# Performance work log

Hardware: AMD Instinct MI355X
Metric: run time of the kernel (lower is better)

The kernel has to match this reference:

```python
import jax, jax.numpy as jnp
import numpy as np

# dims
B, N, T, F, D = 16, 64, 168, 8, 248   # batch, stations, seq, features, gcn_dim
E = D + F                              # transformer dmodel = 256
H = 8                                  # attention heads
FF = 4 * E                             # expansion_factor * dmodel


def _layer_norm(x, g, b, eps=1e-5):
    m = jnp.mean(x, axis=-1, keepdims=True)
    v = jnp.var(x, axis=-1, keepdims=True)
    return (x - m) * jax.lax.rsqrt(v + eps) * g + b


def setup_inputs() -> dict:
    key = jax.random.key(0)
    ks = jax.random.split(key, 20)
    s = 0.02
    return {
        'x': jax.random.normal(ks[0], (B, N, T, F), jnp.float32),
        'locs': jax.random.uniform(ks[1], (B, N, 2), jnp.float32),
        'pos_em': jax.random.normal(ks[2], (B, T, E), jnp.float32),
        'periodic_em': jax.random.normal(ks[3], (B, T, E), jnp.float32),
        'gcn_w': jax.random.normal(ks[4], (F, D), jnp.float32) * s,
        'gcn_b': jnp.zeros((D,), jnp.float32),
        'fc1_w': jax.random.normal(ks[5], (D, D), jnp.float32) * s,
        'fc1_b': jnp.zeros((D,), jnp.float32),
        'wq': jax.random.normal(ks[6], (E, E), jnp.float32) * s,
        'bq': jnp.zeros((E,), jnp.float32),
        'wk': jax.random.normal(ks[7], (E, E), jnp.float32) * s,
        'bk': jnp.zeros((E,), jnp.float32),
        'wv': jax.random.normal(ks[8], (E, E), jnp.float32) * s,
        'bv': jnp.zeros((E,), jnp.float32),
        'wo': jax.random.normal(ks[9], (E, E), jnp.float32) * s,
        'bo': jnp.zeros((E,), jnp.float32),
        'ln1_g': jnp.ones((E,), jnp.float32),
        'ln1_b': jnp.zeros((E,), jnp.float32),
        'ln2_g': jnp.ones((E,), jnp.float32),
        'ln2_b': jnp.zeros((E,), jnp.float32),
        'ff1_w': jax.random.normal(ks[10], (E, FF), jnp.float32) * s,
        'ff1_b': jnp.zeros((FF,), jnp.float32),
        'ff2_w': jax.random.normal(ks[11], (FF, E), jnp.float32) * s,
        'ff2_b': jnp.zeros((E,), jnp.float32),
    }


def reference(x, locs, pos_em, periodic_em, gcn_w, gcn_b, fc1_w, fc1_b,
              wq, bq, wk, bk, wv, bv, wo, bo,
              ln1_g, ln1_b, ln2_g, ln2_b, ff1_w, ff1_b, ff2_w, ff2_b):
    b, n, t, f = x.shape
    # --- inverse-distance-weighted dense adjacency (fully connected graph) ---
    diff = locs[:, :, None, :] - locs[:, None, :, :]            # [B,N,N,2]
    dist = jnp.sqrt(jnp.sum(diff * diff, -1) + 1e-12)           # [B,N,N]
    w = jnp.where(jnp.eye(n, dtype=bool), 0.0, 1.0 / dist)      # no self edges
    w = w / jnp.sum(w, -1, keepdims=True)                       # norm=True
    # --- GCNConv (self loops + symmetric normalization), batched over B and T ---
    a = w + jnp.eye(n, dtype=x.dtype)
    dinv = jax.lax.rsqrt(jnp.sum(a, -1))
    a = a * dinv[:, :, None] * dinv[:, None, :]                 # [B,N,N]
    h = jnp.einsum('bntf,fd->bntd', x, gcn_w)                   # xW
    g = jax.nn.relu(jnp.einsum('bmn,bntd->bmtd', a, h) + gcn_b) # aggregate + relu
    g = jnp.einsum('bntd,de->bnte', g, fc1_w) + fc1_b           # fc1
    # --- concat features, flatten stations into batch, add positional embedding ---
    tok = jnp.concatenate([x, g], -1).reshape(b * n, t, -1)     # [B*N,T,E]
    tok = tok + jnp.repeat(pos_em, n, axis=0)                   # dropout=identity (eval)
    per = jnp.repeat(periodic_em, n, axis=0)
    # --- transformer encoder layer (periodic embedding conditions Q/K) ---
    e = tok.shape[-1]
    dh = e // H
    qk_in = tok + per
    q = (qk_in @ wq + bq).reshape(b * n, t, H, dh)
    k = (qk_in @ wk + bk).reshape(b * n, t, H, dh)
    v = (tok @ wv + bv).reshape(b * n, t, H, dh)
    s = jnp.einsum('bthd,bshd->bhts', q, k) * (1.0 / float(np.sqrt(dh)))
    p = jax.nn.softmax(s, axis=-1)
    o = jnp.einsum('bhts,bshd->bthd', p, v).reshape(b * n, t, e)
    o = o @ wo + bo
    h1 = _layer_norm(tok + o, ln1_g, ln1_b)
    ff = jax.nn.relu(h1 @ ff1_w + ff1_b) @ ff2_w + ff2_b
    out = _layer_norm(h1 + ff, ln2_g, ln2_b)
    return out.reshape(b, n, t, e)
```

## Files before the change

kernel.cpp:

```cpp
#include <hip/hip_runtime.h>
#include <hip/hip_bf16.h>

constexpr int B_  = 16;
constexpr int N_  = 64;
constexpr int T_  = 168;
constexpr int F_  = 8;
constexpr int E_  = 256;
constexpr int H_  = 8;
constexpr int DH_ = 32;
constexpr int NT_ = N_ * T_;
constexpr int LDQ_ = 768;

typedef __bf16 bf16x8 __attribute__((ext_vector_type(8)));
typedef float  f32x4  __attribute__((ext_vector_type(4)));
typedef float  f32x4u __attribute__((ext_vector_type(4), aligned(4)));

__device__ __forceinline__ unsigned short f2b(float f) {
  union { float f; unsigned int u; } v; v.f = f;
  unsigned int r = (v.u + 0x7FFFu + ((v.u >> 16) & 1u)) >> 16;
  return (unsigned short)r;
}
__device__ __forceinline__ float b2f(unsigned short h) {
  union { unsigned int u; float f; } v; v.u = ((unsigned int)h) << 16;
  return v.f;
}
__device__ __forceinline__ unsigned int cvtpk(float lo, float hi) {
  unsigned int r;
  asm("v_cvt_pk_bf16_f32 %0, %1, %2" : "=v"(r) : "v"(lo), "v"(hi));
  return r;
}
__device__ __forceinline__ void gload16(const void* g, void* l) {
  __builtin_amdgcn_global_load_lds(
      (const __attribute__((address_space(1))) unsigned int*)g,
      (__attribute__((address_space(3))) unsigned int*)l, 16, 0, 0);
}

__global__ void adj_kernel(const float* __restrict__ locs, float* __restrict__ a) {
  int b = blockIdx.x;
  int m = threadIdx.x;
  __shared__ float lx[64], ly[64];
  lx[m] = locs[(b * 64 + m) * 2 + 0];
  ly[m] = locs[(b * 64 + m) * 2 + 1];
  __syncthreads();
  float x = lx[m], y = ly[m];
  float sum = 0.f;
  for (int n = 0; n < 64; ++n) {
    float dx = x - lx[n], dy = y - ly[n];
    float d = sqrtf(dx * dx + dy * dy + 1e-12f);
    sum += (n == m) ? 0.f : 1.f / d;
  }
  float inv = 0.5f / sum;
  for (int n = 0; n < 64; ++n) {
    float dx = x - lx[n], dy = y - ly[n];
    float d = sqrtf(dx * dx + dy * dy + 1e-12f);
    float w = (n == m) ? 0.5f : inv / d;
    a[(b * 64 + m) * 64 + n] = w;
  }
}

__global__ void convw_kernel(const float* __restrict__ in, unsigned short* __restrict__ outT,
                             int K, int N, int Kp, int Np) {
  int idx = blockIdx.x * 256 + threadIdx.x;
  if (idx >= Np * Kp) return;
  int n = idx / Kp, k = idx % Kp;
  float v = (k < K && n < N) ? in[(long)k * N + n] : 0.f;
  outT[idx] = f2b(v);
}

__global__ __launch_bounds__(256) void gcn_kernel(
    const float* __restrict__ x, const float* __restrict__ adj,
    const float* __restrict__ gcn_w, const float* __restrict__ gcn_b,
    const float* __restrict__ pos_em, const float* __restrict__ per_em,
    unsigned short* __restrict__ G, unsigned short* __restrict__ tokb,
    unsigned short* __restrict__ qkb, int b0) {
  int bl = blockIdx.x / T_;
  int t = blockIdx.x % T_;
  int b = b0 + bl;
  int tid = threadIdx.x;
  __shared__ float sX[512];
  __shared__ float sXA[512];
  const float* adjb = adj + b * 4096;
  for (int i = tid; i < 512; i += 256) {
    int n = i >> 3, f = i & 7;
    sX[i] = x[((long)(b * 64 + n) * T_ + t) * F_ + f];
  }
  __syncthreads();
  for (int i = tid; i < 512; i += 256) {
    int m = i >> 3, f = i & 7;
    float s = 0.f;
    for (int n = 0; n < 64; ++n) s += adjb[(m << 6) + n] * sX[(n << 3) + f];
    sXA[i] = s;
  }
  {
    long pbase = ((long)bl * T_ + t) * E_;
    for (int i = tid; i < 512; i += 256) {
      int m = i >> 3, f = i & 7;
      long lrow = (long)(bl * 64 + m) * T_ + t;
      float base = sX[i] + pos_em[pbase + f];
      tokb[lrow * E_ + f] = f2b(base);
      qkb[lrow * E_ + f]  = f2b(base + per_em[pbase + f]);
    }
  }
  __syncthreads();
  for (int i = tid; i < 64 * 256; i += 256) {
    int m = i >> 8, d = i & 255;
    float v = 0.f;
    if (d < 248) {
      float s = gcn_b[d];
      const float* xam = &sXA[m << 3];
#pragma unroll
      for (int f = 0; f < 8; ++f) s += xam[f] * gcn_w[f * 248 + d];
      v = fmaxf(s, 0.f);
    }
    long lrow = (long)(bl * 64 + m) * T_ + t;
    G[lrow * 256 + d] = f2b(v);
  }
}

template <int KCHUNKS, int WAVES>
__global__ __launch_bounds__(WAVES * 64) void block_gemm(
    const unsigned short* __restrict__ A, int lda,
    const unsigned short* __restrict__ Bt, int K, int Nact,
    const float* __restrict__ bias,
    float* Cf, unsigned short* Cb1, unsigned short* Cb2,
    const float* __restrict__ emb1, const float* __restrict__ emb2,
    const unsigned short* __restrict__ resb, const float* resf,
    int c0, int ldc, int relu) {
  __shared__ unsigned short As[64 * 256];
  const int tid = threadIdx.x;
  const int lane = tid & 63, w = tid >> 6;
  const int l15 = lane & 15, lg = lane >> 4;
  const int m0 = blockIdx.x * 64;
  const int n0w = blockIdx.y * (WAVES * 64) + w * 64;

  f32x4 acc[4][4];
#pragma unroll
  for (int i = 0; i < 4; ++i)
#pragma unroll
    for (int j = 0; j < 4; ++j) acc[i][j] = (f32x4){0.f, 0.f, 0.f, 0.f};

  for (int kc = 0; kc < KCHUNKS; ++kc) {
    if (kc) __syncthreads();
#pragma unroll
    for (int j = 0; j < 32 / WAVES; ++j) {
      int idx = j * (WAVES * 64) + tid;
      int row = idx >> 5, g = idx & 31;
      int swg = (g & 24) | ((g & 7) ^ (row & 7));
      gload16(A + (long)(m0 + row) * lda + kc * 256 + swg * 8,
              &As[(j * (WAVES * 64) + w * 64) * 8]);
    }
    bf16x8 Wa[4], Wb[4], Xf[4];
    auto ldw = [&](bf16x8 (&W)[4], int ks) {
#pragma unroll
      for (int nf = 0; nf < 4; ++nf)
        W[nf] = *reinterpret_cast<const bf16x8*>(
            Bt + (long)(n0w + nf * 16 + l15) * K + kc * 256 + ks * 32 + (lg << 3));
    };
    auto ldx = [&](int ks) {
#pragma unroll
      for (int mf = 0; mf < 4; ++mf) {
        int row = (mf << 4) + l15;
        int ksg = (ks << 2) + lg;
        int sw = (ksg & 24) | ((ksg & 7) ^ (row & 7));
        Xf[mf] = *reinterpret_cast<const bf16x8*>(&As[((row << 5) + sw) * 8]);
      }
    };
    auto mm = [&](bf16x8 (&W)[4]) {
      __builtin_amdgcn_s_setprio(1);
#pragma unroll
      for (int mf = 0; mf < 4; ++mf)
#pragma unroll
        for (int nf = 0; nf < 4; ++nf)
          acc[mf][nf] = __builtin_amdgcn_mfma_f32_16x16x32_bf16(W[nf], Xf[mf], acc[mf][nf], 0, 0, 0);
      __builtin_amdgcn_s_setprio(0);
    };
    ldw(Wa, 0);
    asm volatile("s_waitcnt vmcnt(0)" ::: "memory");
    __syncthreads();
#pragma unroll
    for (int kp = 0; kp < 4; ++kp) {
      ldw(Wb, kp * 2 + 1);
      ldx(kp * 2);
      mm(Wa);
      if (kp < 3) ldw(Wa, kp * 2 + 2);
      ldx(kp * 2 + 1);
      mm(Wb);
    }
  }

  const int cb = lg << 2;
#pragma unroll
  for (int mf = 0; mf < 4; ++mf) {
    int rr = m0 + (mf << 4) + l15;
    int ar = (rr / NT_) * T_ + (rr % T_);
    long rbase  = (long)rr * ldc + c0;
    long rbase2 = (long)rr * 256 + c0;
    long abase  = (long)ar * 256 + c0;
#pragma unroll
    for (int nf = 0; nf < 4; ++nf) {
      int gcol = n0w + (nf << 4) + cb;
      if (gcol < Nact) {
        float v0 = acc[mf][nf][0], v1 = acc[mf][nf][1];
        float v2 = acc[mf][nf][2], v3 = acc[mf][nf][3];
        if (bias) {
          f32x4u b4 = *reinterpret_cast<const f32x4u*>(bias + gcol);
          v0 += b4[0]; v1 += b4[1]; v2 += b4[2]; v3 += b4[3];
        }
        if (relu) {
          v0 = fmaxf(v0, 0.f); v1 = fmaxf(v1, 0.f);
          v2 = fmaxf(v2, 0.f); v3 = fmaxf(v3, 0.f);
        }
        if (resb) {
          ushort4 rv = *reinterpret_cast<const ushort4*>(resb + rbase2 + gcol);
          v0 += b2f(rv.x); v1 += b2f(rv.y); v2 += b2f(rv.z); v3 += b2f(rv.w);
        }
        if (resf) {
          f32x4u r4 = *reinterpret_cast<const f32x4u*>(resf + rbase + gcol);
          v0 += r4[0]; v1 += r4[1]; v2 += r4[2]; v3 += r4[3];
        }
        if (emb1) {
          f32x4u e4 = *reinterpret_cast<const f32x4u*>(emb1 + abase + gcol);
          v0 += e4[0]; v1 += e4[1]; v2 += e4[2]; v3 += e4[3];
        }
        if (Cf) {
          f32x4u o; o[0] = v0; o[1] = v1; o[2] = v2; o[3] = v3;
          *reinterpret_cast<f32x4u*>(Cf + rbase + gcol) = o;
        }
        if (Cb1) {
          uint2 p = {cvtpk(v0, v1), cvtpk(v2, v3)};
          *reinterpret_cast<uint2*>(Cb1 + rbase + gcol) = p;
        }
        if (Cb2) {
          f32x4u e4 = *reinterpret_cast<const f32x4u*>(emb2 + abase + gcol);
          uint2 p = {cvtpk(v0 + e4[0], v1 + e4[1]), cvtpk(v2 + e4[2], v3 + e4[3])};
          *reinterpret_cast<uint2*>(Cb2 + rbase + gcol) = p;
        }
      }
    }
  }
}

__global__ __launch_bounds__(256) void wo_ln_kernel(
    const unsigned short* __restrict__ A, int lda,
    const unsigned short* __restrict__ Wt,
    const float* __restrict__ bias,
    const unsigned short* __restrict__ resb,
    const float* __restrict__ lng, const float* __restrict__ lnb,
    unsigned short* __restrict__ outb) {
  __shared__ unsigned short As[64 * 256];
  __shared__ float red[4][4][16][2];
  const int tid = threadIdx.x;
  const int lane = tid & 63, w = tid >> 6;
  const int l15 = lane & 15, lg = lane >> 4;
  const int m0 = blockIdx.x * 64;
  const int n0w = w * 64;

  f32x4 acc[4][4];
#pragma unroll
  for (int i = 0; i < 4; ++i)
#pragma unroll
    for (int j = 0; j < 4; ++j) acc[i][j] = (f32x4){0.f, 0.f, 0.f, 0.f};

#pragma unroll
  for (int j = 0; j < 8; ++j) {
    int idx = j * 256 + tid;
    int row = idx >> 5, g = idx & 31;
    int swg = (g & 24) | ((g & 7) ^ (row & 7));
    gload16(A + (long)(m0 + row) * lda + swg * 8, &As[(j * 256 + w * 64) * 8]);
  }
  bf16x8 Wa[4], Wb[4], Xf[4];
  auto ldw = [&](bf16x8 (&W)[4], int ks) {
#pragma unroll
    for (int nf = 0; nf < 4; ++nf)
      W[nf] = *reinterpret_cast<const bf16x8*>(
          Wt + (long)(n0w + nf * 16 + l15) * 256 + ks * 32 + (lg << 3));
  };
  auto ldx = [&](int ks) {
#pragma unroll
    for (int mf = 0; mf < 4; ++mf) {
      int row = (mf << 4) + l15;
      int ksg = (ks << 2) + lg;
      int sw = (ksg & 24) | ((ksg & 7) ^ (row & 7));
      Xf[mf] = *reinterpret_cast<const bf16x8*>(&As[((row << 5) + sw) * 8]);
    }
  };
  auto mm = [&](bf16x8 (&W)[4]) {
    __builtin_amdgcn_s_setprio(1);
#pragma unroll
    for (int mf = 0; mf < 4; ++mf)
// ... 25 lines not shown
#pragma unroll
    for (int nf = 0; nf < 4; ++nf) {
      int gcol = n0w + (nf << 4) + cb;
      f32x4u b4 = *reinterpret_cast<const f32x4u*>(bias + gcol);
      ushort4 rv = *reinterpret_cast<const ushort4*>(resb + rbase2 + gcol);
      float v0 = acc[mf][nf][0] + b4[0] + b2f(rv.x);
      float v1 = acc[mf][nf][1] + b4[1] + b2f(rv.y);
      float v2 = acc[mf][nf][2] + b4[2] + b2f(rv.z);
      float v3 = acc[mf][nf][3] + b4[3] + b2f(rv.w);
      acc[mf][nf][0] = v0; acc[mf][nf][1] = v1;
      acc[mf][nf][2] = v2; acc[mf][nf][3] = v3;
      s[mf] += v0 + v1 + v2 + v3;
      s2[mf] += v0 * v0 + v1 * v1 + v2 * v2 + v3 * v3;
    }
    s[mf] += __shfl_xor(s[mf], 16, 64);
    s[mf] += __shfl_xor(s[mf], 32, 64);
    s2[mf] += __shfl_xor(s2[mf], 16, 64);
    s2[mf] += __shfl_xor(s2[mf], 32, 64);
    if (lg == 0) { red[w][mf][l15][0] = s[mf]; red[w][mf][l15][1] = s2[mf]; }
  }
  __syncthreads();
#pragma unroll
  for (int mf = 0; mf < 4; ++mf) {
    float S  = red[0][mf][l15][0] + red[1][mf][l15][0] + red[2][mf][l15][0] + red[3][mf][l15][0];
    float S2 = red[0][mf][l15][1] + red[1][mf][l15][1] + red[2][mf][l15][1] + red[3][mf][l15][1];
    float mean = S * 0.00390625f;
    float var = S2 * 0.00390625f - mean * mean;
    float rs = rsqrtf(var + 1e-5f);
    int rr = m0 + (mf << 4) + l15;
    long rbase = (long)rr * 256;
#pragma unroll
    for (int nf = 0; nf < 4; ++nf) {
      int gcol = n0w + (nf << 4) + cb;
      f32x4u g4 = *reinterpret_cast<const f32x4u*>(lng + gcol);
      f32x4u t4 = *reinterpret_cast<const f32x4u*>(lnb + gcol);
      float o0 = (acc[mf][nf][0] - mean) * rs * g4[0] + t4[0];
      float o1 = (acc[mf][nf][1] - mean) * rs * g4[1] + t4[1];
      float o2 = (acc[mf][nf][2] - mean) * rs * g4[2] + t4[2];
      float o3 = (acc[mf][nf][3] - mean) * rs * g4[3] + t4[3];
      uint2 p = {cvtpk(o0, o1), cvtpk(o2, o3)};
      *reinterpret_cast<uint2*>(outb + rbase + gcol) = p;
    }
  }
}

__global__ __launch_bounds__(512, 4) void ff_fused_kernel(
    const unsigned short* __restrict__ h1,
    const unsigned short* __restrict__ W1,
    const unsigned short* __restrict__ W2,
    const float* __restrict__ b1, const float* __restrict__ b2,
    const float* __restrict__ lng, const float* __restrict__ lnb,
    float* __restrict__ out) {
  __shared__ unsigned short h1s[64 * 256];
  __shared__ unsigned short fis[64 * 128];
  __shared__ float red[8][4][16][2];
  const int tid = threadIdx.x;
  const int lane = tid & 63, w = tid >> 6;
  const int l15 = lane & 15, lg = lane >> 4;
  const int m0 = blockIdx.x * 64;

#pragma unroll
  for (int j = 0; j < 4; ++j) {
    int idx = j * 512 + tid;
    int row = idx >> 5, g = idx & 31;
    int swg = (g & 24) | ((g & 7) ^ (row & 7));
    gload16(h1 + (long)(m0 + row) * 256 + swg * 8, &h1s[(j * 512 + w * 64) * 8]);
  }

  f32x4 acc2[4][2];
#pragma unroll
  for (int i = 0; i < 4; ++i)
#pragma unroll
    for (int j = 0; j < 2; ++j) acc2[i][j] = (f32x4){0.f, 0.f, 0.f, 0.f};

  bf16x8 W1a, W1b, W2a[2], W2b[2], Xf[4];
  auto ldw1 = [&](bf16x8& W, int hc, int ks) {
    W = *reinterpret_cast<const bf16x8*>(
        W1 + (long)(hc * 128 + w * 16 + l15) * 256 + ks * 32 + (lg << 3));
  };
  auto ldw2 = [&](bf16x8 (&W)[2], int hc, int ks) {
#pragma unroll
    for (int nf = 0; nf < 2; ++nf)
      W[nf] = *reinterpret_cast<const bf16x8*>(
          W2 + (long)(w * 32 + nf * 16 + l15) * 1024 + hc * 128 + ks * 32 + (lg << 3));
  };
  auto ldxh = [&](int ks) {
#pragma unroll
    for (int mf = 0; mf < 4; ++mf) {
      int row = (mf << 4) + l15;
      int ksg = (ks << 2) + lg;
      int sw = (ksg & 24) | ((ksg & 7) ^ (row & 7));
      Xf[mf] = *reinterpret_cast<const bf16x8*>(&h1s[((row << 5) + sw) * 8]);
    }
  };
  auto ldxf = [&](int ks) {
#pragma unroll
    for (int mf = 0; mf < 4; ++mf) {
      int row = (mf << 4) + l15;
      int ksg = (ks << 2) + lg;
      int sw = (ksg & 8) | ((ksg & 7) ^ (row & 7));
      Xf[mf] = *reinterpret_cast<const bf16x8*>(&fis[((row << 4) + sw) * 8]);
    }
  };

  const int cb = lg << 2;
  bool first = true;
  for (int hc = 0; hc < 8; ++hc) {
    f32x4 acc1[4];
#pragma unroll
    for (int i = 0; i < 4; ++i) acc1[i] = (f32x4){0.f, 0.f, 0.f, 0.f};
    ldw1(W1a, hc, 0);
    if (first) {
      asm volatile("s_waitcnt vmcnt(1)" ::: "memory");
      __syncthreads();
      first = false;
    }
#pragma unroll
    for (int kp = 0; kp < 4; ++kp) {
      ldw1(W1b, hc, kp * 2 + 1);
      ldxh(kp * 2);
      __builtin_amdgcn_s_setprio(1);
#pragma unroll
      for (int mf = 0; mf < 4; ++mf)
        acc1[mf] = __builtin_amdgcn_mfma_f32_16x16x32_bf16(W1a, Xf[mf], acc1[mf], 0, 0, 0);
      __builtin_amdgcn_s_setprio(0);
      if (kp < 3) ldw1(W1a, hc, kp * 2 + 2);
      ldxh(kp * 2 + 1);
      __builtin_amdgcn_s_setprio(1);
#pragma unroll
      for (int mf = 0; mf < 4; ++mf)
        acc1[mf] = __builtin_amdgcn_mfma_f32_16x16x32_bf16(W1b, Xf[mf], acc1[mf], 0, 0, 0);
      __builtin_amdgcn_s_setprio(0);
    }
    if (hc) __syncthreads();
#pragma unroll
    for (int mf = 0; mf < 4; ++mf) {
      int row = (mf << 4) + l15;
      int col = w * 16 + cb;
      f32x4u b4 = *reinterpret_cast<const f32x4u*>(b1 + hc * 128 + col);
      float v0 = fmaxf(acc1[mf][0] + b4[0], 0.f);
      float v1 = fmaxf(acc1[mf][1] + b4[1], 0.f);
      float v2 = fmaxf(acc1[mf][2] + b4[2], 0.f);
      float v3 = fmaxf(acc1[mf][3] + b4[3], 0.f);
      int g = col >> 3;
      int swg = (g & 8) | ((g & 7) ^ (row & 7));
      uint2 p = {cvtpk(v0, v1), cvtpk(v2, v3)};
      *reinterpret_cast<uint2*>(&fis[((row << 4) + swg) * 8 + (col & 7)]) = p;
    }
    ldw2(W2a, hc, 0);
    __syncthreads();
#pragma unroll
    for (int kp = 0; kp < 2; ++kp) {
      ldw2(W2b, hc, kp * 2 + 1);
      ldxf(kp * 2);
      __builtin_amdgcn_s_setprio(1);
#pragma unroll
      for (int mf = 0; mf < 4; ++mf)
#pragma unroll
        for (int nf = 0; nf < 2; ++nf)
          acc2[mf][nf] = __builtin_amdgcn_mfma_f32_16x16x32_bf16(W2a[nf], Xf[mf], acc2[mf][nf], 0, 0, 0);
      __builtin_amdgcn_s_setprio(0);
      if (kp < 1) ldw2(W2a, hc, kp * 2 + 2);
      ldxf(kp * 2 + 1);
      __builtin_amdgcn_s_setprio(1);
#pragma unroll
      for (int mf = 0; mf < 4; ++mf)
#pragma unroll
        for (int nf = 0; nf < 2; ++nf)
          acc2[mf][nf] = __builtin_amdgcn_mfma_f32_16x16x32_bf16(W2b[nf], Xf[mf], acc2[mf][nf], 0, 0, 0);
      __builtin_amdgcn_s_setprio(0);
    }
  }

  float s[4], s2[4];
#pragma unroll
  for (int mf = 0; mf < 4; ++mf) {
    int row = (mf << 4) + l15;
    s[mf] = 0.f; s2[mf] = 0.f;
#pragma unroll
    for (int nf = 0; nf < 2; ++nf) {
      int gcol = w * 32 + (nf << 4) + cb;
      f32x4u b4 = *reinterpret_cast<const f32x4u*>(b2 + gcol);
      int g = gcol >> 3;
      int swg = (g & 24) | ((g & 7) ^ (row & 7));
      ushort4 rv = *reinterpret_cast<const ushort4*>(&h1s[((row << 5) + swg) * 8 + (gcol & 7)]);
      float v0 = acc2[mf][nf][0] + b4[0] + b2f(rv.x);
      float v1 = acc2[mf][nf][1] + b4[1] + b2f(rv.y);
      float v2 = acc2[mf][nf][2] + b4[2] + b2f(rv.z);
      float v3 = acc2[mf][nf][3] + b4[3] + b2f(rv.w);
      acc2[mf][nf][0] = v0; acc2[mf][nf][1] = v1;
      acc2[mf][nf][2] = v2; acc2[mf][nf][3] = v3;
      s[mf] += v0 + v1 + v2 + v3;
      s2[mf] += v0 * v0 + v1 * v1 + v2 * v2 + v3 * v3;
    }
    s[mf] += __shfl_xor(s[mf], 16, 64);
    s[mf] += __shfl_xor(s[mf], 32, 64);
    s2[mf] += __shfl_xor(s2[mf], 16, 64);
    s2[mf] += __shfl_xor(s2[mf], 32, 64);
    if (lg == 0) { red[w][mf][l15][0] = s[mf]; red[w][mf][l15][1] = s2[mf]; }
  }
  __syncthreads();
#pragma unroll
  for (int mf = 0; mf < 4; ++mf) {
    float S = 0.f, S2 = 0.f;
#pragma unroll
    for (int ww = 0; ww < 8; ++ww) { S += red[ww][mf][l15][0]; S2 += red[ww][mf][l15][1]; }
    float mean = S * 0.00390625f;
    float var = S2 * 0.00390625f - mean * mean;
    float rs = rsqrtf(var + 1e-5f);
    int rr = m0 + (mf << 4) + l15;
    long rbase = (long)rr * 256;
#pragma unroll
    for (int nf = 0; nf < 2; ++nf) {
      int gcol = w * 32 + (nf << 4) + cb;
      f32x4u g4 = *reinterpret_cast<const f32x4u*>(lng + gcol);
      f32x4u t4 = *reinterpret_cast<const f32x4u*>(lnb + gcol);
      f32x4u o;
      o[0] = (acc2[mf][nf][0] - mean) * rs * g4[0] + t4[0];
      o[1] = (acc2[mf][nf][1] - mean) * rs * g4[1] + t4[1];
      o[2] = (acc2[mf][nf][2] - mean) * rs * g4[2] + t4[2];
      o[3] = (acc2[mf][nf][3] - mean) * rs * g4[3] + t4[3];
      *reinterpret_cast<f32x4u*>(out + rbase + gcol) = o;
    }
// ... 82 lines not shown
    f32x4 o0 = (f32x4){0.f, 0.f, 0.f, 0.f};
    f32x4 o1 = (f32x4){0.f, 0.f, 0.f, 0.f};
#pragma unroll
    for (int ks = 0; ks < 6; ++ks) {
      bf16x8 pf = *reinterpret_cast<const bf16x8*>(&Pw[l15 * 200 + ks * 32 + (lg << 3)]);
      bf16x8 v0 = *reinterpret_cast<const bf16x8*>(&VT[l15][ks * 32 + (lg << 3)]);
      bf16x8 v1 = *reinterpret_cast<const bf16x8*>(&VT[16 + l15][ks * 32 + (lg << 3)]);
      o0 = __builtin_amdgcn_mfma_f32_16x16x32_bf16(pf, v0, o0, 0, 0, 0);
      o1 = __builtin_amdgcn_mfma_f32_16x16x32_bf16(pf, v1, o1, 0, 0, 0);
    }
    int rg = lg << 2;
#pragma unroll
    for (int r = 0; r < 4; ++r) {
      int q = qt * 16 + rg + r;
      if (q < T_) {
        long ob = (long)q * LDQ_;
        O[ob + l15]      = f2b(o0[r] * inv_l[r]);
        O[ob + 16 + l15] = f2b(o1[r] * inv_l[r]);
      }
    }
  }
}

extern "C" void kernel_launch(void* const* d_in, const int* in_sizes, int n_in,
                              void* d_out, int out_size, void* d_ws, size_t ws_size,
                              hipStream_t stream) {
  const float* x      = (const float*)d_in[0];
  const float* locs   = (const float*)d_in[1];
  const float* pos_em = (const float*)d_in[2];
  const float* per_em = (const float*)d_in[3];
  const float* gcn_w  = (const float*)d_in[4];
  const float* gcn_b  = (const float*)d_in[5];
  const float* fc1_w  = (const float*)d_in[6];
  const float* fc1_b  = (const float*)d_in[7];
  const float* wq = (const float*)d_in[8];
  const float* bq = (const float*)d_in[9];
  const float* wk = (const float*)d_in[10];
  const float* bk = (const float*)d_in[11];
  const float* wv = (const float*)d_in[12];
  const float* bv = (const float*)d_in[13];
  const float* wo = (const float*)d_in[14];
  const float* bo = (const float*)d_in[15];
  const float* ln1_g = (const float*)d_in[16];
  const float* ln1_b = (const float*)d_in[17];
  const float* ln2_g = (const float*)d_in[18];
  const float* ln2_b = (const float*)d_in[19];
  const float* ff1_w = (const float*)d_in[20];
  const float* ff1_b = (const float*)d_in[21];
  const float* ff2_w = (const float*)d_in[22];
  const float* ff2_b = (const float*)d_in[23];
  float* out = (float*)d_out;

  const size_t ADJ_BYTES = 1u << 20;
  const size_t WB_BYTES  = 2u << 20;
  int CB = 16;
  while (CB > 1) {
    if (ADJ_BYTES + WB_BYTES + (size_t)CB * NT_ * 2560 <= ws_size) break;
    CB >>= 1;
  }
  char* ws = (char*)d_ws;
  float* adj = (float*)ws;
  unsigned short* wslab = (unsigned short*)(ws + ADJ_BYTES);
  unsigned short* fc1T  = wslab;
  unsigned short* wqkT  = wslab + 65536;
  unsigned short* wkT   = wslab + 2 * 65536;
  unsigned short* wvT   = wslab + 3 * 65536;
  unsigned short* woT   = wslab + 4 * 65536;
  unsigned short* ff1T  = wslab + 5 * 65536;
  unsigned short* ff2T  = wslab + 5 * 65536 + 262144;
  float* bqk = (float*)(ws + ADJ_BYTES + 1900544);

  unsigned short* tokb = (unsigned short*)(ws + ADJ_BYTES + WB_BYTES);
  unsigned short* qkb  = tokb + (size_t)CB * NT_ * 256;
  unsigned short* qkv  = qkb + (size_t)CB * NT_ * 256;
  unsigned short* h1b  = tokb;

  adj_kernel<<<B_, 64, 0, stream>>>(locs, adj);
  convw_kernel<<<256, 256, 0, stream>>>(fc1_w, fc1T, 248, 248, 256, 256);
  convw_kernel<<<256, 256, 0, stream>>>(wq, wqkT, 256, 256, 256, 256);
  convw_kernel<<<256, 256, 0, stream>>>(wk, wkT, 256, 256, 256, 256);
  convw_kernel<<<256, 256, 0, stream>>>(wv, wvT, 256, 256, 256, 256);
  convw_kernel<<<256, 256, 0, stream>>>(wo, woT, 256, 256, 256, 256);
  convw_kernel<<<1024, 256, 0, stream>>>(ff1_w, ff1T, 256, 1024, 256, 1024);
  convw_kernel<<<1024, 256, 0, stream>>>(ff2_w, ff2T, 1024, 256, 1024, 256);
  hipMemcpyAsync(bqk, bq, 256 * sizeof(float), hipMemcpyDeviceToDevice, stream);
  hipMemcpyAsync(bqk + 256, bk, 256 * sizeof(float), hipMemcpyDeviceToDevice, stream);

  for (int b0 = 0; b0 < B_; b0 += CB) {
    const int rows = CB * NT_;
    const int GX = rows / 64;
    const float* pos_c = pos_em + (long)b0 * T_ * E_;
    const float* per_c = per_em + (long)b0 * T_ * E_;
    float* out_c = out + (long)b0 * NT_ * E_;
    unsigned short* G = qkv;

    gcn_kernel<<<CB * T_, 256, 0, stream>>>(x, adj, gcn_w, gcn_b, pos_c, per_c,
                                            G, tokb, qkb, b0);
    block_gemm<1, 4><<<dim3(GX, 1), 256, 0, stream>>>(
        G, 256, fc1T, 256, 248, fc1_b, nullptr, tokb, qkb, pos_c, per_c,
        nullptr, nullptr, 8, 256, 0);
    block_gemm<1, 8><<<dim3(GX, 1), 512, 0, stream>>>(
        qkb, 256, wqkT, 256, 512, bqk, nullptr, qkv, nullptr, nullptr, nullptr,
        nullptr, nullptr, 0, LDQ_, 0);
    block_gemm<1, 4><<<dim3(GX, 1), 256, 0, stream>>>(
        tokb, 256, wvT, 256, 256, bv, nullptr, qkv, nullptr, nullptr, nullptr,
        nullptr, nullptr, 512, LDQ_, 0);
    attn_mfma_kernel<<<CB * N_ * H_, 256, 0, stream>>>(qkv);
    wo_ln_kernel<<<GX, 256, 0, stream>>>(qkv, LDQ_, woT, bo, tokb,
                                         ln1_g, ln1_b, h1b);
    ff_fused_kernel<<<GX, 512, 0, stream>>>(h1b, ff1T, ff2T, ff1_b, ff2_b,
                                            ln2_g, ln2_b, out_c);
  }
}
```

Baseline: 1.153 ms.

## Double-buffer FF intermediate tile to overlap first and second GEMM stages

The fused feed-forward kernel now keeps two LDS buffers for the ReLU intermediate. It computes the next hidden chunk's first GEMM while running the second GEMM on the current chunk, which cuts the per-chunk barriers from two to one. The goal is to hide latency by interleaving independent MFMA work between the two GEMMs. In exchange it uses an extra 16KB of LDS, raises register pressure from the live accumulators, and fully unrolls the loop, so occupancy may drop.

Result: no change. 1.173 ms (median of 2 runs) (+1.7%).

```diff
diff --git a/kernel.cpp b/kernel.cpp
--- a/kernel.cpp
+++ b/kernel.cpp
@@ -366,12 +366,14 @@
     const float* __restrict__ lng, const float* __restrict__ lnb,
     float* __restrict__ out) {
   __shared__ unsigned short h1s[64 * 256];
-  __shared__ unsigned short fis[64 * 128];
+  __shared__ unsigned short fisA[64 * 128];
+  __shared__ unsigned short fisB[64 * 128];
   __shared__ float red[8][4][16][2];
   const int tid = threadIdx.x;
   const int lane = tid & 63, w = tid >> 6;
   const int l15 = lane & 15, lg = lane >> 4;
   const int m0 = blockIdx.x * 64;
+  const int cb = lg << 2;
 
 #pragma unroll
   for (int j = 0; j < 4; ++j) {
@@ -380,6 +382,8 @@
     int swg = (g & 24) | ((g & 7) ^ (row & 7));
     gload16(h1 + (long)(m0 + row) * 256 + swg * 8, &h1s[(j * 512 + w * 64) * 8]);
   }
+  asm volatile("s_waitcnt vmcnt(0)" ::: "memory");
+  __syncthreads();
 
   f32x4 acc2[4][2];
 #pragma unroll
@@ -387,102 +391,97 @@
 #pragma unroll
     for (int j = 0; j < 2; ++j) acc2[i][j] = (f32x4){0.f, 0.f, 0.f, 0.f};
 
-  bf16x8 W1a, W1b, W2a[2], W2b[2], Xf[4];
   auto ldw1 = [&](bf16x8& W, int hc, int ks) {
     W = *reinterpret_cast<const bf16x8*>(
         W1 + (long)(hc * 128 + w * 16 + l15) * 256 + ks * 32 + (lg << 3));
   };
-  auto ldw2 = [&](bf16x8 (&W)[2], int hc, int ks) {
-#pragma unroll
-    for (int nf = 0; nf < 2; ++nf)
-      W[nf] = *reinterpret_cast<const bf16x8*>(
-          W2 + (long)(w * 32 + nf * 16 + l15) * 1024 + hc * 128 + ks * 32 + (lg << 3));
+  auto stage1 = [&](f32x4 (&a1)[4], int hc) {
+#pragma unroll
+    for (int i = 0; i < 4; ++i) a1[i] = (f32x4){0.f, 0.f, 0.f, 0.f};
+    bf16x8 Wa, Wb, Xf[4];
+    auto ldxh = [&](int ks) {
+#pragma unroll
+      for (int mf = 0; mf < 4; ++mf) {
+        int row = (mf << 4) + l15;
+        int ksg = (ks << 2) + lg;
+        int sw = (ksg & 24) | ((ksg & 7) ^ (row & 7));
+        Xf[mf] = *reinterpret_cast<const bf16x8*>(&h1s[((row << 5) + sw) * 8]);
+      }
+    };
+    ldw1(Wa, hc, 0);
+#pragma unroll
+    for (int kp = 0; kp < 4; ++kp) {
+      ldw1(Wb, hc, kp * 2 + 1);
+      ldxh(kp * 2);
+      __builtin_amdgcn_s_setprio(1);
+#pragma unroll
+      for (int mf = 0; mf < 4; ++mf)
+        a1[mf] = __builtin_amdgcn_mfma_f32_16x16x32_bf16(Wa, Xf[mf], a1[mf], 0, 0, 0);
+      __builtin_amdgcn_s_setprio(0);
+      if (kp < 3) ldw1(Wa, hc, kp * 2 + 2);
+      ldxh(kp * 2 + 1);
+      __builtin_amdgcn_s_setprio(1);
+#pragma unroll
+      for (int mf = 0; mf < 4; ++mf)
+        a1[mf] = __builtin_amdgcn_mfma_f32_16x16x32_bf16(Wb, Xf[mf], a1[mf], 0, 0, 0);
+      __builtin_amdgcn_s_setprio(0);
+    }
   };
-  auto ldxh = [&](int ks) {
+  auto stage2 = [&](const unsigned short* fis, int hc) {
+    bf16x8 Wf[2], Xf[4];
+#pragma unroll
+    for (int ks = 0; ks < 4; ++ks) {
+#pragma unroll
+      for (int nf = 0; nf < 2; ++nf)
+        Wf[nf] = *reinterpret_cast<const bf16x8*>(
+            W2 + (long)(w * 32 + nf * 16 + l15) * 1024 + hc * 128 + ks * 32 + (lg << 3));
+#pragma unroll
+      for (int mf = 0; mf < 4; ++mf) {
+        int row = (mf << 4) + l15;
+        int ksg = (ks << 2) + lg;
+        int sw = (ksg & 8) | ((ksg & 7) ^ (row & 7));
+        Xf[mf] = *reinterpret_cast<const bf16x8*>(&fis[((row << 4) + sw) * 8]);
+      }
+      __builtin_amdgcn_s_setprio(1);
+#pragma unroll
+      for (int mf = 0; mf < 4; ++mf)
+#pragma unroll
+        for (int nf = 0; nf < 2; ++nf)
+          acc2[mf][nf] = __builtin_amdgcn_mfma_f32_16x16x32_bf16(Wf[nf], Xf[mf], acc2[mf][nf], 0, 0, 0);
+      __builtin_amdgcn_s_setprio(0);
+    }
+  };
+  auto writeFis = [&](unsigned short* fis, f32x4 (&a1)[4], int hc) {
+    int col = w * 16 + cb;
+    f32x4u b4 = *reinterpret_cast<const f32x4u*>(b1 + hc * 128 + col);
+    int g = col >> 3;
 #pragma unroll
     for (int mf = 0; mf < 4; ++mf) {
       int row = (mf << 4) + l15;
-      int ksg = (ks << 2) + lg;
-      int sw = (ksg & 24) | ((ksg & 7) ^ (row & 7));
-      Xf[mf] = *reinterpret_cast<const bf16x8*>(&h1s[((row << 5) + sw) * 8]);
-    }
-  };
-  auto ldxf = [&](int ks) {
-#pragma unroll
-    for (int mf = 0; mf < 4; ++mf) {
-      int row = (mf << 4) + l15;
-      int ksg = (ks << 2) + lg;
-      int sw = (ksg & 8) | ((ksg & 7) ^ (row & 7));
-      Xf[mf] = *reinterpret_cast<const bf16x8*>(&fis[((row << 4) + sw) * 8]);
-    }
-  };
-
-  const int cb = lg << 2;
-  bool first = true;
-  for (int hc = 0; hc < 8; ++hc) {
-    f32x4 acc1[4];
-#pragma unroll
-    for (int i = 0; i < 4; ++i) acc1[i] = (f32x4){0.f, 0.f, 0.f, 0.f};
-    ldw1(W1a, hc, 0);
-    if (first) {
-      asm volatile("s_waitcnt vmcnt(1)" ::: "memory");
-      __syncthreads();
-      first = false;
-    }
-#pragma unroll
-    for (int kp = 0; kp < 4; ++kp) {
-      ldw1(W1b, hc, kp * 2 + 1);
-      ldxh(kp * 2);
-      __builtin_amdgcn_s_setprio(1);
-#pragma unroll
-      for (int mf = 0; mf < 4; ++mf)
-        acc1[mf] = __builtin_amdgcn_mfma_f32_16x16x32_bf16(W1a, Xf[mf], acc1[mf], 0, 0, 0);
-      __builtin_amdgcn_s_setprio(0);
-      if (kp < 3) ldw1(W1a, hc, kp * 2 + 2);
-      ldxh(kp * 2 + 1);
-      __builtin_amdgcn_s_setprio(1);
-#pragma unroll
-      for (int mf = 0; mf < 4; ++mf)
-        acc1[mf] = __builtin_amdgcn_mfma_f32_16x16x32_bf16(W1b, Xf[mf], acc1[mf], 0, 0, 0);
-      __builtin_amdgcn_s_setprio(0);
-    }
-    if (hc) __syncthreads();
-#pragma unroll
-    for (int mf = 0; mf < 4; ++mf) {
-      int row = (mf << 4) + l15;
-      int col = w * 16 + cb;
-      f32x4u b4 = *reinterpret_cast<const f32x4u*>(b1 + hc * 128 + col);
-      float v0 = fmaxf(acc1[mf][0] + b4[0], 0.f);
-      float v1 = fmaxf(acc1[mf][1] + b4[1], 0.f);
-      float v2 = fmaxf(acc1[mf][2] + b4[2], 0.f);
-      float v3 = fmaxf(acc1[mf][3] + b4[3], 0.f);
-      int g = col >> 3;
+      float v0 = fmaxf(a1[mf][0] + b4[0], 0.f);
+      float v1 = fmaxf(a1[mf][1] + b4[1], 0.f);
+      float v2 = fmaxf(a1[mf][2] + b4[2], 0.f);
+      float v3 = fmaxf(a1[mf][3] + b4[3], 0.f);
       int swg = (g & 8) | ((g & 7) ^ (row & 7));
       uint2 p = {cvtpk(v0, v1), cvtpk(v2, v3)};
       *reinterpret_cast<uint2*>(&fis[((row << 4) + swg) * 8 + (col & 7)]) = p;
     }
-    ldw2(W2a, hc, 0);
-    __syncthreads();
-#pragma unroll
-    for (int kp = 0; kp < 2; ++kp) {
-      ldw2(W2b, hc, kp * 2 + 1);
-      ldxf(kp * 2);
-      __builtin_amdgcn_s_setprio(1);
-#pragma unroll
-      for (int mf = 0; mf < 4; ++mf)
-#pragma unroll
-        for (int nf = 0; nf < 2; ++nf)
-          acc2[mf][nf] = __builtin_amdgcn_mfma_f32_16x16x32_bf16(W2a[nf], Xf[mf], acc2[mf][nf], 0, 0, 0);
-      __builtin_amdgcn_s_setprio(0);
-      if (kp < 1) ldw2(W2a, hc, kp * 2 + 2);
-      ldxf(kp * 2 + 1);
-      __builtin_amdgcn_s_setprio(1);
-#pragma unroll
-      for (int mf = 0; mf < 4; ++mf)
-#pragma unroll
-        for (int nf = 0; nf < 2; ++nf)
-          acc2[mf][nf] = __builtin_amdgcn_mfma_f32_16x16x32_bf16(W2b[nf], Xf[mf], acc2[mf][nf], 0, 0, 0);
-      __builtin_amdgcn_s_setprio(0);
+  };
+
+  f32x4 a1[4];
+  stage1(a1, 0);
+  writeFis(fisA, a1, 0);
+  __syncthreads();
+
+#pragma unroll
+  for (int hc = 0; hc < 8; ++hc) {
+    const unsigned short* rdp = (hc & 1) ? fisB : fisA;
+    unsigned short* wrp = (hc & 1) ? fisA : fisB;
+    if (hc < 7) stage1(a1, hc + 1);
+    stage2(rdp, hc);
+    if (hc < 7) {
+      writeFis(wrp, a1, hc + 1);
+      __syncthreads();
     }
   }
 
```

## Precompute periodic-embedding QK projection once per time step; restructure FF loop

Applied to the files above, without the earlier changes.

Uses linearity, (tok+per)Wq = tok·Wq + per·Wq, to compute per·[Wq|Wk]+bias once over B*T rows instead of B*N*T rows. The result is added as an fp32 embedding in the QK GEMM epilogue, which removes the separate qkb buffer and its writes. The fused FF kernel now processes two 128-wide hidden chunks per iteration with double-buffered LDS, halving the number of barriers. This adds an extra fp32 read of the perq table per QK output and more registers and LDS in the FF kernel.

New measurement: 1.197 ms. +3.8%, slower.

```diff
diff --git a/kernel.cpp b/kernel.cpp
--- a/kernel.cpp
+++ b/kernel.cpp
@@ -10,6 +10,7 @@
 constexpr int DH_ = 32;
 constexpr int NT_ = N_ * T_;
 constexpr int LDQ_ = 768;
+constexpr int BT_ = B_ * T_;
 
 typedef __bf16 bf16x8 __attribute__((ext_vector_type(8)));
 typedef float  f32x4  __attribute__((ext_vector_type(4)));
@@ -67,12 +68,17 @@
   outT[idx] = f2b(v);
 }
 
+__global__ void cvtb_kernel(const float* __restrict__ in, unsigned short* __restrict__ out,
+                            int n) {
+  int i = blockIdx.x * 256 + threadIdx.x;
+  if (i < n) out[i] = f2b(in[i]);
+}
+
 __global__ __launch_bounds__(256) void gcn_kernel(
     const float* __restrict__ x, const float* __restrict__ adj,
     const float* __restrict__ gcn_w, const float* __restrict__ gcn_b,
-    const float* __restrict__ pos_em, const float* __restrict__ per_em,
-    unsigned short* __restrict__ G, unsigned short* __restrict__ tokb,
-    unsigned short* __restrict__ qkb, int b0) {
+    const float* __restrict__ pos_em,
+    unsigned short* __restrict__ G, unsigned short* __restrict__ tokb, int b0) {
   int bl = blockIdx.x / T_;
   int t = blockIdx.x % T_;
   int b = b0 + bl;
@@ -96,9 +102,7 @@
     for (int i = tid; i < 512; i += 256) {
       int m = i >> 3, f = i & 7;
       long lrow = (long)(bl * 64 + m) * T_ + t;
-      float base = sX[i] + pos_em[pbase + f];
-      tokb[lrow * E_ + f] = f2b(base);
-      qkb[lrow * E_ + f]  = f2b(base + per_em[pbase + f]);
+      tokb[lrow * E_ + f] = f2b(sX[i] + pos_em[pbase + f]);
     }
   }
   __syncthreads();
@@ -122,10 +126,10 @@
     const unsigned short* __restrict__ A, int lda,
     const unsigned short* __restrict__ Bt, int K, int Nact,
     const float* __restrict__ bias,
-    float* Cf, unsigned short* Cb1, unsigned short* Cb2,
-    const float* __restrict__ emb1, const float* __restrict__ emb2,
+    float* Cf, unsigned short* Cb1,
+    const float* __restrict__ emb1,
     const unsigned short* __restrict__ resb, const float* resf,
-    int c0, int ldc, int relu) {
+    int c0, int ldc, int lde, int relu) {
   __shared__ unsigned short As[64 * 256];
   const int tid = threadIdx.x;
   const int lane = tid & 63, w = tid >> 6;
@@ -195,7 +199,7 @@
     int ar = (rr / NT_) * T_ + (rr % T_);
     long rbase  = (long)rr * ldc + c0;
     long rbase2 = (long)rr * 256 + c0;
-    long abase  = (long)ar * 256 + c0;
+    long abase  = (long)ar * lde + c0;
 #pragma unroll
     for (int nf = 0; nf < 4; ++nf) {
       int gcol = n0w + (nf << 4) + cb;
@@ -230,11 +234,6 @@
           uint2 p = {cvtpk(v0, v1), cvtpk(v2, v3)};
           *reinterpret_cast<uint2*>(Cb1 + rbase + gcol) = p;
         }
-        if (Cb2) {
-          f32x4u e4 = *reinterpret_cast<const f32x4u*>(emb2 + abase + gcol);
-          uint2 p = {cvtpk(v0 + e4[0], v1 + e4[1]), cvtpk(v2 + e4[2], v3 + e4[3])};
-          *reinterpret_cast<uint2*>(Cb2 + rbase + gcol) = p;
-        }
       }
     }
   }
@@ -366,12 +365,13 @@
     const float* __restrict__ lng, const float* __restrict__ lnb,
     float* __restrict__ out) {
   __shared__ unsigned short h1s[64 * 256];
-  __shared__ unsigned short fis[64 * 128];
+  __shared__ unsigned short fis[2][64 * 128];
   __shared__ float red[8][4][16][2];
   const int tid = threadIdx.x;
   const int lane = tid & 63, w = tid >> 6;
   const int l15 = lane & 15, lg = lane >> 4;
   const int m0 = blockIdx.x * 64;
+  const int cb = lg << 2;
 
 #pragma unroll
   for (int j = 0; j < 4; ++j) {
@@ -387,10 +387,13 @@
 #pragma unroll
     for (int j = 0; j < 2; ++j) acc2[i][j] = (f32x4){0.f, 0.f, 0.f, 0.f};
 
-  bf16x8 W1a, W1b, W2a[2], W2b[2], Xf[4];
-  auto ldw1 = [&](bf16x8& W, int hc, int ks) {
-    W = *reinterpret_cast<const bf16x8*>(
-        W1 + (long)(hc * 128 + w * 16 + l15) * 256 + ks * 32 + (lg << 3));
+  bf16x8 W1a[2], W1b[2], W2a[2], W2b[2], Xf[4];
+  f32x4 acc1[4][2];
+  auto ldw1 = [&](bf16x8 (&W)[2], int p, int ks) {
+#pragma unroll
+    for (int c = 0; c < 2; ++c)
+      W[c] = *reinterpret_cast<const bf16x8*>(
+          W1 + (long)((2 * p + c) * 128 + w * 16 + l15) * 256 + ks * 32 + (lg << 3));
   };
   auto ldw2 = [&](bf16x8 (&W)[2], int hc, int ks) {
 #pragma unroll
@@ -407,82 +410,87 @@
       Xf[mf] = *reinterpret_cast<const bf16x8*>(&h1s[((row << 5) + sw) * 8]);
     }
   };
-  auto ldxf = [&](int ks) {
-#pragma unroll
-    for (int mf = 0; mf < 4; ++mf) {
-      int row = (mf << 4) + l15;
-      int ksg = (ks << 2) + lg;
-      int sw = (ksg & 8) | ((ksg & 7) ^ (row & 7));
-      Xf[mf] = *reinterpret_cast<const bf16x8*>(&fis[((row << 4) + sw) * 8]);
-    }
+  auto mm1 = [&](bf16x8 (&W)[2]) {
+    __builtin_amdgcn_s_setprio(1);
+#pragma unroll
+    for (int mf = 0; mf < 4; ++mf)
+#pragma unroll
+      for (int c = 0; c < 2; ++c)
+        acc1[mf][c] = __builtin_amdgcn_mfma_f32_16x16x32_bf16(W[c], Xf[mf], acc1[mf][c], 0, 0, 0);
+    __builtin_amdgcn_s_setprio(0);
   };
-
-  const int cb = lg << 2;
+  auto mm2 = [&](bf16x8 (&W)[2]) {
+    __builtin_amdgcn_s_setprio(1);
+#pragma unroll
+    for (int mf = 0; mf < 4; ++mf)
+#pragma unroll
+      for (int nf = 0; nf < 2; ++nf)
+        acc2[mf][nf] = __builtin_amdgcn_mfma_f32_16x16x32_bf16(W[nf], Xf[mf], acc2[mf][nf], 0, 0, 0);
+    __builtin_amdgcn_s_setprio(0);
+  };
+
   bool first = true;
-  for (int hc = 0; hc < 8; ++hc) {
-    f32x4 acc1[4];
-#pragma unroll
-    for (int i = 0; i < 4; ++i) acc1[i] = (f32x4){0.f, 0.f, 0.f, 0.f};
-    ldw1(W1a, hc, 0);
+#pragma unroll
+  for (int p = 0; p < 4; ++p) {
+#pragma unroll
+    for (int i = 0; i < 4; ++i)
+#pragma unroll
+      for (int c = 0; c < 2; ++c) acc1[i][c] = (f32x4){0.f, 0.f, 0.f, 0.f};
+    ldw1(W1a, p, 0);
     if (first) {
-      asm volatile("s_waitcnt vmcnt(1)" ::: "memory");
+      asm volatile("s_waitcnt vmcnt(2)" ::: "memory");
       __syncthreads();
       first = false;
     }
 #pragma unroll
     for (int kp = 0; kp < 4; ++kp) {
-      ldw1(W1b, hc, kp * 2 + 1);
+      ldw1(W1b, p, kp * 2 + 1);
       ldxh(kp * 2);
-      __builtin_amdgcn_s_setprio(1);
-#pragma unroll
-      for (int mf = 0; mf < 4; ++mf)
-        acc1[mf] = __builtin_amdgcn_mfma_f32_16x16x32_bf16(W1a, Xf[mf], acc1[mf], 0, 0, 0);
-      __builtin_amdgcn_s_setprio(0);
-      if (kp < 3) ldw1(W1a, hc, kp * 2 + 2);
+      mm1(W1a);
+      if (kp < 3) ldw1(W1a, p, kp * 2 + 2);
       ldxh(kp * 2 + 1);
-      __builtin_amdgcn_s_setprio(1);
-#pragma unroll
-      for (int mf = 0; mf < 4; ++mf)
-        acc1[mf] = __builtin_amdgcn_mfma_f32_16x16x32_bf16(W1b, Xf[mf], acc1[mf], 0, 0, 0);
-      __builtin_amdgcn_s_setprio(0);
-    }
-    if (hc) __syncthreads();
-#pragma unroll
-    for (int mf = 0; mf < 4; ++mf) {
-      int row = (mf << 4) + l15;
+      mm1(W1b);
+    }
+    if (p) __syncthreads();
+#pragma unroll
+    for (int c = 0; c < 2; ++c) {
       int col = w * 16 + cb;
-      f32x4u b4 = *reinterpret_cast<const f32x4u*>(b1 + hc * 128 + col);
-      float v0 = fmaxf(acc1[mf][0] + b4[0], 0.f);
-      float v1 = fmaxf(acc1[mf][1] + b4[1], 0.f);
-      float v2 = fmaxf(acc1[mf][2] + b4[2], 0.f);
-      float v3 = fmaxf(acc1[mf][3] + b4[3], 0.f);
+      f32x4u b4 = *reinterpret_cast<const f32x4u*>(b1 + (2 * p + c) * 128 + col);
       int g = col >> 3;
-      int swg = (g & 8) | ((g & 7) ^ (row & 7));
-      uint2 p = {cvtpk(v0, v1), cvtpk(v2, v3)};
-      *reinterpret_cast<uint2*>(&fis[((row << 4) + swg) * 8 + (col & 7)]) = p;
-    }
-    ldw2(W2a, hc, 0);
+#pragma unroll
+      for (int mf = 0; mf < 4; ++mf) {
+        int row = (mf << 4) + l15;
+        float v0 = fmaxf(acc1[mf][c][0] + b4[0], 0.f);
+        float v1 = fmaxf(acc1[mf][c][1] + b4[1], 0.f);
+        float v2 = fmaxf(acc1[mf][c][2] + b4[2], 0.f);
+        float v3 = fmaxf(acc1[mf][c][3] + b4[3], 0.f);
+        int swg = (g & 8) | ((g & 7) ^ (row & 7));
+        uint2 pk = {cvtpk(v0, v1), cvtpk(v2, v3)};
+        *reinterpret_cast<uint2*>(&fis[c][((row << 4) + swg) * 8 + (col & 7)]) = pk;
+      }
+    }
+    ldw2(W2a, 2 * p, 0);
     __syncthreads();
 #pragma unroll
-    for (int kp = 0; kp < 2; ++kp) {
-      ldw2(W2b, hc, kp * 2 + 1);
-      ldxf(kp * 2);
-      __builtin_amdgcn_s_setprio(1);
-#pragma unroll
-      for (int mf = 0; mf < 4; ++mf)
-#pragma unroll
-        for (int nf = 0; nf < 2; ++nf)
-          acc2[mf][nf] = __builtin_amdgcn_mfma_f32_16x16x32_bf16(W2a[nf], Xf[mf], acc2[mf][nf], 0, 0, 0);
-      __builtin_amdgcn_s_setprio(0);
-      if (kp < 1) ldw2(W2a, hc, kp * 2 + 2);
-      ldxf(kp * 2 + 1);
-      __builtin_amdgcn_s_setprio(1);
-#pragma unroll
-      for (int mf = 0; mf < 4; ++mf)
-#pragma unroll
-        for (int nf = 0; nf < 2; ++nf)
-          acc2[mf][nf] = __builtin_amdgcn_mfma_f32_16x16x32_bf16(W2b[nf], Xf[mf], acc2[mf][nf], 0, 0, 0);
-      __builtin_amdgcn_s_setprio(0);
+    for (int c = 0; c < 2; ++c) {
+      int hc = 2 * p + c;
+      auto ldxf = [&](int ks) {
+#pragma unroll
+        for (int mf = 0; mf < 4; ++mf) {
+          int row = (mf << 4) + l15;
+          int ksg = (ks << 2) + lg;
+          int sw = (ksg & 8) | ((ksg & 7) ^ (row & 7));
+          Xf[mf] = *reinterpret_cast<const bf16x8*>(&fis[c][((row << 4) + sw) * 8]);
+        }
+      };
+      ldw2(W2b, hc, 1);
+      ldxf(0); mm2(W2a);
+      ldw2(W2a, hc, 2);
+      ldxf(1); mm2(W2b);
+      ldw2(W2b, hc, 3);
+      ldxf(2); mm2(W2a);
+      if (c == 0) ldw2(W2a, 2 * p + 1, 0);
+      ldxf(3); mm2(W2b);
     }
   }
 
@@ -671,10 +679,10 @@
   float* out = (float*)d_out;
 
   const size_t ADJ_BYTES = 1u << 20;
-  const size_t WB_BYTES  = 2u << 20;
+  const size_t WB_BYTES  = 16u << 20;
   int CB = 16;
   while (CB > 1) {
-    if (ADJ_BYTES + WB_BYTES + (size_t)CB * NT_ * 2560 <= ws_size) break;
+    if (ADJ_BYTES + WB_BYTES + (size_t)CB * NT_ * 2048 <= ws_size) break;
     CB >>= 1;
   }
   char* ws = (char*)d_ws;
@@ -688,10 +696,11 @@
   unsigned short* ff1T  = wslab + 5 * 65536;
   unsigned short* ff2T  = wslab + 5 * 65536 + 262144;
   float* bqk = (float*)(ws + ADJ_BYTES + 1900544);
+  unsigned short* perb = (unsigned short*)(ws + ADJ_BYTES + (2u << 20));
+  float* perq = (float*)(ws + ADJ_BYTES + (4u << 20));
 
   unsigned short* tokb = (unsigned short*)(ws + ADJ_BYTES + WB_BYTES);
-  unsigned short* qkb  = tokb + (size_t)CB * NT_ * 256;
-  unsigned short* qkv  = qkb + (size_t)CB * NT_ * 256;
+  unsigned short* qkv  = tokb + (size_t)CB * NT_ * 256;
   unsigned short* h1b  = tokb;
 
   adj_kernel<<<B_, 64, 0, stream>>>(locs, adj);
@@ -702,28 +711,32 @@
   convw_kernel<<<256, 256, 0, stream>>>(wo, woT, 256, 256, 256, 256);
   convw_kernel<<<1024, 256, 0, stream>>>(ff1_w, ff1T, 256, 1024, 256, 1024);
   convw_kernel<<<1024, 256, 0, stream>>>(ff2_w, ff2T, 1024, 256, 1024, 256);
+  cvtb_kernel<<<BT_, 256, 0, stream>>>(per_em, perb, BT_ * 256);
   hipMemcpyAsync(bqk, bq, 256 * sizeof(float), hipMemcpyDeviceToDevice, stream);
   hipMemcpyAsync(bqk + 256, bk, 256 * sizeof(float), hipMemcpyDeviceToDevice, stream);
+  block_gemm<1, 8><<<dim3(BT_ / 64, 1), 512, 0, stream>>>(
+      perb, 256, wqkT, 256, 512, bqk, perq, nullptr, nullptr,
+      nullptr, nullptr, 0, 512, 256, 0);
 
   for (int b0 = 0; b0 < B_; b0 += CB) {
     const int rows = CB * NT_;
     const int GX = rows / 64;
     const float* pos_c = pos_em + (long)b0 * T_ * E_;
-    const float* per_c = per_em + (long)b0 * T_ * E_;
+    const float* perq_c = perq + (long)b0 * T_ * 512;
     float* out_c = out + (long)b0 * NT_ * E_;
     unsigned short* G = qkv;
 
-    gcn_kernel<<<CB * T_, 256, 0, stream>>>(x, adj, gcn_w, gcn_b, pos_c, per_c,
-                                            G, tokb, qkb, b0);
+    gcn_kernel<<<CB * T_, 256, 0, stream>>>(x, adj, gcn_w, gcn_b, pos_c,
+                                            G, tokb, b0);
     block_gemm<1, 4><<<dim3(GX, 1), 256, 0, stream>>>(
-        G, 256, fc1T, 256, 248, fc1_b, nullptr, tokb, qkb, pos_c, per_c,
-        nullptr, nullptr, 8, 256, 0);
+        G, 256, fc1T, 256, 248, fc1_b, nullptr, tokb, pos_c,
+        nullptr, nullptr, 8, 256, 256, 0);
     block_gemm<1, 8><<<dim3(GX, 1), 512, 0, stream>>>(
-        qkb, 256, wqkT, 256, 512, bqk, nullptr, qkv, nullptr, nullptr, nullptr,
-        nullptr, nullptr, 0, LDQ_, 0);
+        tokb, 256, wqkT, 256, 512, nullptr, nullptr, qkv, perq_c,
+        nullptr, nullptr, 0, LDQ_, 512, 0);
     block_gemm<1, 4><<<dim3(GX, 1), 256, 0, stream>>>(
-        tokb, 256, wvT, 256, 256, bv, nullptr, qkv, nullptr, nullptr, nullptr,
-        nullptr, nullptr, 512, LDQ_, 0);
+        tokb, 256, wvT, 256, 256, bv, nullptr, qkv, nullptr,
+        nullptr, nullptr, 512, LDQ_, 256, 0);
     attn_mfma_kernel<<<CB * N_ * H_, 256, 0, stream>>>(qkv);
     wo_ln_kernel<<<GX, 256, 0, stream>>>(qkv, LDQ_, woT, bo, tokb,
                                          ln1_g, ln1_b, h1b);
```

## Precompute periodic-embedding Q/K projection once per batch and add in epilogue

Applied to the files above, without the earlier changes.

Uses linearity, (tok+per)@Wqk = tok@Wqk + per@Wqk. The periodic embedding's Q/K projection is computed once over B*T rows instead of over B*N*T rows, and is then added as an fp32 embedding term in the QK GEMM epilogue. This removes the separate qkb bf16 buffer, its writes from gcn and fc1, and a full activation read. It costs an extra small GEMM and a strided fp32 read of perq in the epilogue. Rounding also differs slightly because per is no longer summed in bf16 before the GEMM.

Measured after the change: 1.095 ms. 1.05x faster.

```diff
diff --git a/kernel.cpp b/kernel.cpp
--- a/kernel.cpp
+++ b/kernel.cpp
@@ -10,6 +10,7 @@
 constexpr int DH_ = 32;
 constexpr int NT_ = N_ * T_;
 constexpr int LDQ_ = 768;
+constexpr int BT_ = B_ * T_;
 
 typedef __bf16 bf16x8 __attribute__((ext_vector_type(8)));
 typedef float  f32x4  __attribute__((ext_vector_type(4)));
@@ -67,12 +68,17 @@
   outT[idx] = f2b(v);
 }
 
+__global__ void cvtb_kernel(const float* __restrict__ in, unsigned short* __restrict__ out,
+                            int n) {
+  int i = blockIdx.x * 256 + threadIdx.x;
+  if (i < n) out[i] = f2b(in[i]);
+}
+
 __global__ __launch_bounds__(256) void gcn_kernel(
     const float* __restrict__ x, const float* __restrict__ adj,
     const float* __restrict__ gcn_w, const float* __restrict__ gcn_b,
-    const float* __restrict__ pos_em, const float* __restrict__ per_em,
-    unsigned short* __restrict__ G, unsigned short* __restrict__ tokb,
-    unsigned short* __restrict__ qkb, int b0) {
+    const float* __restrict__ pos_em,
+    unsigned short* __restrict__ G, unsigned short* __restrict__ tokb, int b0) {
   int bl = blockIdx.x / T_;
   int t = blockIdx.x % T_;
   int b = b0 + bl;
@@ -96,9 +102,7 @@
     for (int i = tid; i < 512; i += 256) {
       int m = i >> 3, f = i & 7;
       long lrow = (long)(bl * 64 + m) * T_ + t;
-      float base = sX[i] + pos_em[pbase + f];
-      tokb[lrow * E_ + f] = f2b(base);
-      qkb[lrow * E_ + f]  = f2b(base + per_em[pbase + f]);
+      tokb[lrow * E_ + f] = f2b(sX[i] + pos_em[pbase + f]);
     }
   }
   __syncthreads();
@@ -122,10 +126,10 @@
     const unsigned short* __restrict__ A, int lda,
     const unsigned short* __restrict__ Bt, int K, int Nact,
     const float* __restrict__ bias,
-    float* Cf, unsigned short* Cb1, unsigned short* Cb2,
-    const float* __restrict__ emb1, const float* __restrict__ emb2,
+    float* Cf, unsigned short* Cb1,
+    const float* __restrict__ emb1,
     const unsigned short* __restrict__ resb, const float* resf,
-    int c0, int ldc, int relu) {
+    int c0, int ldc, int lde, int relu) {
   __shared__ unsigned short As[64 * 256];
   const int tid = threadIdx.x;
   const int lane = tid & 63, w = tid >> 6;
@@ -195,7 +199,7 @@
     int ar = (rr / NT_) * T_ + (rr % T_);
     long rbase  = (long)rr * ldc + c0;
     long rbase2 = (long)rr * 256 + c0;
-    long abase  = (long)ar * 256 + c0;
+    long abase  = (long)ar * lde + c0;
 #pragma unroll
     for (int nf = 0; nf < 4; ++nf) {
       int gcol = n0w + (nf << 4) + cb;
@@ -230,11 +234,6 @@
           uint2 p = {cvtpk(v0, v1), cvtpk(v2, v3)};
           *reinterpret_cast<uint2*>(Cb1 + rbase + gcol) = p;
         }
-        if (Cb2) {
-          f32x4u e4 = *reinterpret_cast<const f32x4u*>(emb2 + abase + gcol);
-          uint2 p = {cvtpk(v0 + e4[0], v1 + e4[1]), cvtpk(v2 + e4[2], v3 + e4[3])};
-          *reinterpret_cast<uint2*>(Cb2 + rbase + gcol) = p;
-        }
       }
     }
   }
@@ -671,10 +670,10 @@
   float* out = (float*)d_out;
 
   const size_t ADJ_BYTES = 1u << 20;
-  const size_t WB_BYTES  = 2u << 20;
+  const size_t WB_BYTES  = 16u << 20;
   int CB = 16;
   while (CB > 1) {
-    if (ADJ_BYTES + WB_BYTES + (size_t)CB * NT_ * 2560 <= ws_size) break;
+    if (ADJ_BYTES + WB_BYTES + (size_t)CB * NT_ * 2048 <= ws_size) break;
     CB >>= 1;
   }
   char* ws = (char*)d_ws;
@@ -688,10 +687,11 @@
   unsigned short* ff1T  = wslab + 5 * 65536;
   unsigned short* ff2T  = wslab + 5 * 65536 + 262144;
   float* bqk = (float*)(ws + ADJ_BYTES + 1900544);
+  unsigned short* perb = (unsigned short*)(ws + ADJ_BYTES + (2u << 20));
+  float* perq = (float*)(ws + ADJ_BYTES + (4u << 20));
 
   unsigned short* tokb = (unsigned short*)(ws + ADJ_BYTES + WB_BYTES);
-  unsigned short* qkb  = tokb + (size_t)CB * NT_ * 256;
-  unsigned short* qkv  = qkb + (size_t)CB * NT_ * 256;
+  unsigned short* qkv  = tokb + (size_t)CB * NT_ * 256;
   unsigned short* h1b  = tokb;
 
   adj_kernel<<<B_, 64, 0, stream>>>(locs, adj);
@@ -702,28 +702,32 @@
   convw_kernel<<<256, 256, 0, stream>>>(wo, woT, 256, 256, 256, 256);
   convw_kernel<<<1024, 256, 0, stream>>>(ff1_w, ff1T, 256, 1024, 256, 1024);
   convw_kernel<<<1024, 256, 0, stream>>>(ff2_w, ff2T, 1024, 256, 1024, 256);
+  cvtb_kernel<<<BT_, 256, 0, stream>>>(per_em, perb, BT_ * 256);
   hipMemcpyAsync(bqk, bq, 256 * sizeof(float), hipMemcpyDeviceToDevice, stream);
   hipMemcpyAsync(bqk + 256, bk, 256 * sizeof(float), hipMemcpyDeviceToDevice, stream);
+  block_gemm<1, 8><<<dim3(BT_ / 64, 1), 512, 0, stream>>>(
+      perb, 256, wqkT, 256, 512, bqk, perq, nullptr, nullptr,
+      nullptr, nullptr, 0, 512, 256, 0);
 
   for (int b0 = 0; b0 < B_; b0 += CB) {
     const int rows = CB * NT_;
     const int GX = rows / 64;
     const float* pos_c = pos_em + (long)b0 * T_ * E_;
-    const float* per_c = per_em + (long)b0 * T_ * E_;
+    const float* perq_c = perq + (long)b0 * T_ * 512;
     float* out_c = out + (long)b0 * NT_ * E_;
     unsigned short* G = qkv;
 
-    gcn_kernel<<<CB * T_, 256, 0, stream>>>(x, adj, gcn_w, gcn_b, pos_c, per_c,
-                                            G, tokb, qkb, b0);
+    gcn_kernel<<<CB * T_, 256, 0, stream>>>(x, adj, gcn_w, gcn_b, pos_c,
+                                            G, tokb, b0);
     block_gemm<1, 4><<<dim3(GX, 1), 256, 0, stream>>>(
-        G, 256, fc1T, 256, 248, fc1_b, nullptr, tokb, qkb, pos_c, per_c,
-        nullptr, nullptr, 8, 256, 0);
+        G, 256, fc1T, 256, 248, fc1_b, nullptr, tokb, pos_c,
+        nullptr, nullptr, 8, 256, 256, 0);
     block_gemm<1, 8><<<dim3(GX, 1), 512, 0, stream>>>(
-        qkb, 256, wqkT, 256, 512, bqk, nullptr, qkv, nullptr, nullptr, nullptr,
-        nullptr, nullptr, 0, LDQ_, 0);
+        tokb, 256, wqkT, 256, 512, nullptr, nullptr, qkv, perq_c,
+        nullptr, nullptr, 0, LDQ_, 512, 0);
     block_gemm<1, 4><<<dim3(GX, 1), 256, 0, stream>>>(
-        tokb, 256, wvT, 256, 256, bv, nullptr, qkv, nullptr, nullptr, nullptr,
-        nullptr, nullptr, 512, LDQ_, 0);
+        tokb, 256, wvT, 256, 256, bv, nullptr, qkv, nullptr,
+        nullptr, nullptr, 512, LDQ_, 256, 0);
     attn_mfma_kernel<<<CB * N_ * H_, 256, 0, stream>>>(qkv);
     wo_ln_kernel<<<GX, 256, 0, stream>>>(qkv, LDQ_, woT, bo, tokb,
                                          ln1_g, ln1_b, h1b);
```
